# Performance work log

Hardware: AMD Instinct MI355X
Metric: run time of the kernel (lower is better)

## Reference

```python
import jax, jax.numpy as jnp
import numpy as np

N_NODES = 1024      # nNodes
N_EDGES = 4096      # nEdges
N_FACTORS = 64      # input feature dim (rows of kernel / paths)
BATCH = 256
NNZ_PER_ROW = 32    # nonzeros per kernel row -> iter = count_nonzero = 32 exactly
N_SOURCES = 16


def setup_inputs() -> dict:
    key = jax.random.key(0)
    k1, k2 = jax.random.split(key, 2)
    x = jax.random.normal(k1, (BATCH, N_FACTORS), dtype=jnp.float32)

    rng = np.random.default_rng(0)
    lin = rng.choice(N_NODES * N_NODES, size=N_EDGES, replace=False)
    # Edges[e] = (col, row): original scatters node_prop[i, Edges[e][1], Edges[e][0]] = paths[i][e]
    edges = np.stack([lin % N_NODES, lin // N_NODES], axis=1).astype(np.int64)

    sources = np.sort(rng.choice(N_NODES, size=N_SOURCES, replace=False)).astype(np.int64)

    # kernel ("paths") with exactly NNZ_PER_ROW nonzeros per row, so the
    # data-dependent propagation depth count_nonzero(paths[i]) == NNZ_PER_ROW
    cols = np.argsort(rng.random((N_FACTORS, N_EDGES)), axis=1)[:, :NNZ_PER_ROW]
    mask = np.zeros((N_FACTORS, N_EDGES), dtype=np.float32)
    mask[np.arange(N_FACTORS)[:, None], cols] = 1.0
    dense = np.asarray(jax.random.normal(k2, (N_FACTORS, N_EDGES), dtype=jnp.float32)) * 0.1
    kernel = jnp.asarray(dense * mask)

    return {
        "x": x,
        "kernel": kernel,
        "edges": jnp.asarray(edges),
        "sources": jnp.asarray(sources),
    }


def reference(x, kernel, edges, sources):
    F, E = kernel.shape
    N = N_NODES

    # scatter-build per-factor adjacency: node_prop[i, dst, src] = kernel[i, e]
    node_prop = jnp.zeros((F, N, N), x.dtype).at[:, edges[:, 1], edges[:, 0]].set(kernel)
    # row 0 fixed so each column sums to 1
    node_prop = node_prop.at[:, 0, :].set(1.0 - node_prop.sum(axis=1))

    source_flow = jnp.zeros((N,), x.dtype).at[sources].set(1.0)

    # data-dependent propagation depth per factor
    iters = jnp.count_nonzero(kernel, axis=1)  # [F], == NNZ_PER_ROW by construction

    # prop_flow[i] is linear in factor[i]; propagate the unit source vector per factor
    V0 = jnp.broadcast_to(source_flow, (F, N))

    def step(V, t):
        Vn = jnp.einsum('fij,fj->fi', node_prop, V)
        return jnp.where(t < iters[:, None], Vn, V), None

    V, _ = jax.lax.scan(step, V0, jnp.arange(NNZ_PER_ROW))

    # subtract factor[i] at every source node: W[i] = V[i] - 1_{sources}
    W = V - source_flow  # [F, N]

    prop_flows = x @ W        # [B, N]  (sum over factors of scaled propagated flows)
    recon = x @ kernel        # [B, E]  linear-combination reconstruction
    return prop_flows, recon
```

## Files before the change

### kernel.cpp

```cpp
#include <hip/hip_runtime.h>
#include <hip/hip_bf16.h>

#define NNODES   1024
#define NEDGES   4096
#define NFACT    64
#define NBATCH   256
#define NSRC     16
#define MAXNNZ   64
#define MAXITER  32

#define RECON_BLOCKS 512
#define FLOWS_BLOCKS 128

__global__ __launch_bounds__(256) void k1(
    const float* __restrict__ kern,
    const int*   __restrict__ edges,
    const int*   __restrict__ sources,
    const float* __restrict__ x,
    float*       __restrict__ W,
    float*       __restrict__ out)
{
    if (blockIdx.x >= NFACT) {
        int r  = blockIdx.x - NFACT;
        int e4 = (r & 3) * 256 + threadIdx.x;
        int b0 = (r >> 2) * 2;
        const float4* Kv  = (const float4*)kern;
        const float*  xr0 = x + b0 * NFACT;
        const float*  xr1 = xr0 + NFACT;
        float4 a0 = {0.f,0.f,0.f,0.f}, a1 = {0.f,0.f,0.f,0.f};
        #pragma unroll 4
        for (int k = 0; k < NFACT; ++k) {
            float4 kv = Kv[k * (NEDGES/4) + e4];
            float x0 = xr0[k], x1 = xr1[k];
            a0.x += x0*kv.x; a0.y += x0*kv.y; a0.z += x0*kv.z; a0.w += x0*kv.w;
            a1.x += x1*kv.x; a1.y += x1*kv.y; a1.z += x1*kv.z; a1.w += x1*kv.w;
        }
        float4* o4 = (float4*)(out + NBATCH * NNODES);
        o4[ b0      * (NEDGES/4) + e4] = a0;
        o4[(b0 + 1) * (NEDGES/4) + e4] = a1;
        return;
    }

    __shared__ float v_lds[NNODES];
    __shared__ float wbuf[MAXNNZ];
    __shared__ int   srcbuf[MAXNNZ];
    __shared__ int   dstbuf[MAXNNZ];
    __shared__ float c_lds[MAXNNZ];
    __shared__ int   cnt;

    const int f = blockIdx.x;
    const int t = threadIdx.x;

    if (t == 0) cnt = 0;
    __syncthreads();

    const float4* kern4 = (const float4*)(kern + f * NEDGES);
    #pragma unroll
    for (int i = 0; i < NEDGES/4/256; ++i) {
        int e4 = t + i * 256;
        float4 kv = kern4[e4];
        float vals[4] = {kv.x, kv.y, kv.z, kv.w};
        #pragma unroll
        for (int c = 0; c < 4; ++c) {
            if (vals[c] != 0.f) {
                int slot = atomicAdd(&cnt, 1);
                if (slot < MAXNNZ) {
                    wbuf[slot]   = vals[c];
                    int e        = e4 * 4 + c;
                    srcbuf[slot] = edges[2*e];
                    dstbuf[slot] = edges[2*e + 1];
                }
            }
        }
    }
    __syncthreads();

    const int nnz = min(cnt, MAXNNZ);
    const int T   = min(nnz, MAXITER);

    for (int n = t; n < NNODES; n += 256) v_lds[n] = 0.f;
    __syncthreads();

    if (t < 64) {
        const bool  active = (t < nnz);
        const float w_e = active ? wbuf[t]   : 0.f;
        const int   src = active ? srcbuf[t] : -1;
        const int   dst = active ? dstbuf[t] : -1;

        unsigned long long gmask = 0ull;
        for (int e2 = 0; e2 < nnz; ++e2)
            if (dstbuf[e2] == src) gmask |= (1ull << e2);

        float val = 0.f;
        for (int s = 0; s < NSRC; ++s)
            if (sources[s] == src) val = 1.f;
        float S = (float)NSRC;

        unsigned long long anybad =
            __ballot(active && (src == 0 || dst == 0)) |
            __ballot(__popcll(gmask) > 1);

        if (T > 0) {
            float c_fin = 0.f, v0_fin = 0.f;
            if (anybad == 0ull) {
                const int   gidx = gmask ? (__ffsll(gmask) - 1) : t;
                const float gsel = gmask ? 1.f : 0.f;
                float c = 0.f;
                for (int it = 0; it < T; ++it) {
                    c = w_e * val;
                    float g = __shfl(c, gidx);
                    val = gsel * g;
                }
                float a = c;
                #pragma unroll
                for (int o = 32; o >= 1; o >>= 1) a += __shfl_xor(a, o);
                c_fin = c; v0_fin = S - a;
            } else {
                float c = 0.f, v0 = 0.f;
                for (int it = 0; it < T; ++it) {
                    c = w_e * val;
                    c_lds[t] = c;
                    float a = c;
                    float b = (dst == 0) ? c : 0.f;
                    #pragma unroll
                    for (int o = 32; o >= 1; o >>= 1) {
                        a += __shfl_xor(a, o);
                        b += __shfl_xor(b, o);
                    }
                    v0 = S - a;
                    S  = S - b;
                    float nv = 0.f;
                    unsigned long long m = gmask;
                    while (m) { int i = __ffsll(m) - 1; nv += c_lds[i]; m &= m - 1; }
                    val = (src == 0) ? v0 : nv;
                }
                c_fin = c; v0_fin = v0;
            }
            if (t == 0) v_lds[0] = v0_fin;
            if (active && dst != 0) atomicAdd(&v_lds[dst], c_fin);
        } else {
            if (t < NSRC) v_lds[sources[t]] = 1.f;
        }
    }
    __syncthreads();
    if (t < NSRC) atomicAdd(&v_lds[sources[t]], -1.f);
    __syncthreads();

    float4* Wr = (float4*)(W + f * NNODES);
    const float4* v4 = (const float4*)v_lds;
    Wr[t] = v4[t];
}

__global__ __launch_bounds__(256) void k2(
    const float* __restrict__ x,
    const float* __restrict__ W,
    float*       __restrict__ out)
{
    const int b0 = blockIdx.x * 2;
    const int t  = threadIdx.x;
    const float4* Wv  = (const float4*)W;
    const float*  xr0 = x + b0 * NFACT;
    const float*  xr1 = xr0 + NFACT;
    float4 a0 = {0.f,0.f,0.f,0.f}, a1 = {0.f,0.f,0.f,0.f};
    #pragma unroll 4
    for (int k = 0; k < NFACT; ++k) {
        float4 wv = Wv[k * (NNODES/4) + t];
        float x0 = xr0[k], x1 = xr1[k];
        a0.x += x0*wv.x; a0.y += x0*wv.y; a0.z += x0*wv.z; a0.w += x0*wv.w;
        a1.x += x1*wv.x; a1.y += x1*wv.y; a1.z += x1*wv.z; a1.w += x1*wv.w;
    }
    float4* o4 = (float4*)out;
    o4[ b0      * (NNODES/4) + t] = a0;
    o4[(b0 + 1) * (NNODES/4) + t] = a1;
}

extern "C" void kernel_launch(void* const* d_in, const int* in_sizes, int n_in,
                              void* d_out, int out_size, void* d_ws, size_t ws_size,
                              hipStream_t stream) {
    const float* x       = (const float*)d_in[0];
    const float* kern    = (const float*)d_in[1];
    const int*   edges   = (const int*)d_in[2];
    const int*   sources = (const int*)d_in[3];
    float* out = (float*)d_out;
    float* W   = (float*)d_ws;

    k1<<<NFACT + RECON_BLOCKS, 256, 0, stream>>>(kern, edges, sources, x, W, out);
    k2<<<FLOWS_BLOCKS, 256, 0, stream>>>(x, W, out);
}
```

Before: 83.11 us.

## Fuse propagation, recon and flows into one kernel with flag-based inter-block sync

Merges the two launches into one grid. The propagation blocks publish each W row and then set a per-factor release flag. The flows blocks spin with acquire loads on those flags before computing x @ W. This removes the second kernel launch and the serialization between the two kernels. Recon and flows blocks now each handle four batch rows, with x staged in LDS, which halves the block counts. The flags are never reset, so on repeated calls the flows blocks may not wait and could read W while it is being rewritten. The spin-wait also relies on all blocks being co-resident.

```diff
diff --git a/kernel.cpp b/kernel.cpp
--- a/kernel.cpp
+++ b/kernel.cpp
@@ -9,169 +9,192 @@
 #define MAXNNZ   64
 #define MAXITER  32
 
-#define RECON_BLOCKS 512
-#define FLOWS_BLOCKS 128
-
-__global__ __launch_bounds__(256) void k1(
+#define PROP_BLOCKS  64
+#define RECON_BLOCKS 256
+#define FLOWS_BLOCKS 64
+#define GRID_BLOCKS  (PROP_BLOCKS + RECON_BLOCKS + FLOWS_BLOCKS)
+
+__global__ __launch_bounds__(256, 4) void fused(
     const float* __restrict__ kern,
     const int*   __restrict__ edges,
     const int*   __restrict__ sources,
     const float* __restrict__ x,
-    float*       __restrict__ W,
+    float*       __restrict__ ws,
     float*       __restrict__ out)
 {
-    if (blockIdx.x >= NFACT) {
-        int r  = blockIdx.x - NFACT;
-        int e4 = (r & 3) * 256 + threadIdx.x;
-        int b0 = (r >> 2) * 2;
-        const float4* Kv  = (const float4*)kern;
-        const float*  xr0 = x + b0 * NFACT;
-        const float*  xr1 = xr0 + NFACT;
-        float4 a0 = {0.f,0.f,0.f,0.f}, a1 = {0.f,0.f,0.f,0.f};
-        #pragma unroll 4
-        for (int k = 0; k < NFACT; ++k) {
-            float4 kv = Kv[k * (NEDGES/4) + e4];
-            float x0 = xr0[k], x1 = xr1[k];
-            a0.x += x0*kv.x; a0.y += x0*kv.y; a0.z += x0*kv.z; a0.w += x0*kv.w;
-            a1.x += x1*kv.x; a1.y += x1*kv.y; a1.z += x1*kv.z; a1.w += x1*kv.w;
-        }
-        float4* o4 = (float4*)(out + NBATCH * NNODES);
-        o4[ b0      * (NEDGES/4) + e4] = a0;
-        o4[(b0 + 1) * (NEDGES/4) + e4] = a1;
-        return;
-    }
-
     __shared__ float v_lds[NNODES];
+    __shared__ float xs[256];
     __shared__ float wbuf[MAXNNZ];
     __shared__ int   srcbuf[MAXNNZ];
     __shared__ int   dstbuf[MAXNNZ];
     __shared__ float c_lds[MAXNNZ];
     __shared__ int   cnt;
 
-    const int f = blockIdx.x;
-    const int t = threadIdx.x;
-
-    if (t == 0) cnt = 0;
-    __syncthreads();
-
-    const float4* kern4 = (const float4*)(kern + f * NEDGES);
-    #pragma unroll
-    for (int i = 0; i < NEDGES/4/256; ++i) {
-        int e4 = t + i * 256;
-        float4 kv = kern4[e4];
-        float vals[4] = {kv.x, kv.y, kv.z, kv.w};
+    const int bid = blockIdx.x;
+    const int t   = threadIdx.x;
+    float* W      = ws;
+    int*   flags  = (int*)(ws + NFACT * NNODES);
+
+    if (bid < PROP_BLOCKS) {
+        const int f = bid;
+        if (t == 0) cnt = 0;
+        __syncthreads();
+
+        const float4* kern4 = (const float4*)(kern + f * NEDGES);
         #pragma unroll
-        for (int c = 0; c < 4; ++c) {
-            if (vals[c] != 0.f) {
-                int slot = atomicAdd(&cnt, 1);
-                if (slot < MAXNNZ) {
-                    wbuf[slot]   = vals[c];
-                    int e        = e4 * 4 + c;
-                    srcbuf[slot] = edges[2*e];
-                    dstbuf[slot] = edges[2*e + 1];
+        for (int i = 0; i < NEDGES/4/256; ++i) {
+            int e4 = t + i * 256;
+            float4 kv = kern4[e4];
+            float vals[4] = {kv.x, kv.y, kv.z, kv.w};
+            #pragma unroll
+            for (int c = 0; c < 4; ++c) {
+                if (vals[c] != 0.f) {
+                    int slot = atomicAdd(&cnt, 1);
+                    if (slot < MAXNNZ) {
+                        wbuf[slot]   = vals[c];
+                        int e        = e4 * 4 + c;
+                        srcbuf[slot] = edges[2*e];
+                        dstbuf[slot] = edges[2*e + 1];
+                    }
                 }
             }
         }
+        __syncthreads();
+
+        const int nnz = min(cnt, MAXNNZ);
+        const int T   = min(nnz, MAXITER);
+
+        for (int n = t; n < NNODES; n += 256) v_lds[n] = 0.f;
+        __syncthreads();
+
+        if (t < 64) {
+            const bool  active = (t < nnz);
+            const float w_e = active ? wbuf[t]   : 0.f;
+            const int   src = active ? srcbuf[t] : -1;
+            const int   dst = active ? dstbuf[t] : -1;
+
+            unsigned long long gmask = 0ull;
+            for (int e2 = 0; e2 < nnz; ++e2)
+                if (dstbuf[e2] == src) gmask |= (1ull << e2);
+
+            float val = 0.f;
+            for (int s = 0; s < NSRC; ++s)
+                if (sources[s] == src) val = 1.f;
+            float S = (float)NSRC;
+
+            unsigned long long anybad =
+                __ballot(active && (src == 0 || dst == 0)) |
+                __ballot(__popcll(gmask) > 1);
+
+            if (T > 0) {
+                float c_fin = 0.f, v0_fin = 0.f;
+                if (anybad == 0ull) {
+                    const int   gidx = gmask ? (__ffsll(gmask) - 1) : t;
+                    const float gsel = gmask ? 1.f : 0.f;
+                    float c = 0.f;
+                    for (int it = 0; it < T; ++it) {
+                        c = w_e * val;
+                        float g = __shfl(c, gidx);
+                        val = gsel * g;
+                    }
+                    float a = c;
+                    #pragma unroll
+                    for (int o = 32; o >= 1; o >>= 1) a += __shfl_xor(a, o);
+                    c_fin = c; v0_fin = S - a;
+                } else {
+                    float c = 0.f, v0 = 0.f;
+                    for (int it = 0; it < T; ++it) {
+                        c = w_e * val;
+                        c_lds[t] = c;
+                        float a = c;
+                        float b = (dst == 0) ? c : 0.f;
+                        #pragma unroll
+                        for (int o = 32; o >= 1; o >>= 1) {
+                            a += __shfl_xor(a, o);
+                            b += __shfl_xor(b, o);
+                        }
+                        v0 = S - a;
+                        S  = S - b;
+                        float nv = 0.f;
+                        unsigned long long m = gmask;
+                        while (m) { int i = __ffsll(m) - 1; nv += c_lds[i]; m &= m - 1; }
+                        val = (src == 0) ? v0 : nv;
+                    }
+                    c_fin = c; v0_fin = v0;
+                }
+                if (t == 0) v_lds[0] = v0_fin;
+                if (active && dst != 0) atomicAdd(&v_lds[dst], c_fin);
+            } else {
+                if (t < NSRC) v_lds[sources[t]] = 1.f;
+            }
+        }
+        __syncthreads();
+        if (t < NSRC) atomicAdd(&v_lds[sources[t]], -1.f);
+        __syncthreads();
+
+        ((float4*)(W + f * NNODES))[t] = ((const float4*)v_lds)[t];
+        __syncthreads();
+        if (t == 0) {
+            __threadfence();
+            __hip_atomic_store(&flags[f], 1, __ATOMIC_RELEASE, __HIP_MEMORY_SCOPE_AGENT);
+        }
+        return;
     }
-    __syncthreads();
-
-    const int nnz = min(cnt, MAXNNZ);
-    const int T   = min(nnz, MAXITER);
-
-    for (int n = t; n < NNODES; n += 256) v_lds[n] = 0.f;
-    __syncthreads();
-
-    if (t < 64) {
-        const bool  active = (t < nnz);
-        const float w_e = active ? wbuf[t]   : 0.f;
-        const int   src = active ? srcbuf[t] : -1;
-        const int   dst = active ? dstbuf[t] : -1;
-
-        unsigned long long gmask = 0ull;
-        for (int e2 = 0; e2 < nnz; ++e2)
-            if (dstbuf[e2] == src) gmask |= (1ull << e2);
-
-        float val = 0.f;
-        for (int s = 0; s < NSRC; ++s)
-            if (sources[s] == src) val = 1.f;
-        float S = (float)NSRC;
-
-        unsigned long long anybad =
-            __ballot(active && (src == 0 || dst == 0)) |
-            __ballot(__popcll(gmask) > 1);
-
-        if (T > 0) {
-            float c_fin = 0.f, v0_fin = 0.f;
-            if (anybad == 0ull) {
-                const int   gidx = gmask ? (__ffsll(gmask) - 1) : t;
-                const float gsel = gmask ? 1.f : 0.f;
-                float c = 0.f;
-                for (int it = 0; it < T; ++it) {
-                    c = w_e * val;
-                    float g = __shfl(c, gidx);
-                    val = gsel * g;
-                }
-                float a = c;
-                #pragma unroll
-                for (int o = 32; o >= 1; o >>= 1) a += __shfl_xor(a, o);
-                c_fin = c; v0_fin = S - a;
-            } else {
-                float c = 0.f, v0 = 0.f;
-                for (int it = 0; it < T; ++it) {
-                    c = w_e * val;
-                    c_lds[t] = c;
-                    float a = c;
-                    float b = (dst == 0) ? c : 0.f;
-                    #pragma unroll
-                    for (int o = 32; o >= 1; o >>= 1) {
-                        a += __shfl_xor(a, o);
-                        b += __shfl_xor(b, o);
-                    }
-                    v0 = S - a;
-                    S  = S - b;
-                    float nv = 0.f;
-                    unsigned long long m = gmask;
-                    while (m) { int i = __ffsll(m) - 1; nv += c_lds[i]; m &= m - 1; }
-                    val = (src == 0) ? v0 : nv;
-                }
-                c_fin = c; v0_fin = v0;
-            }
-            if (t == 0) v_lds[0] = v0_fin;
-            if (active && dst != 0) atomicAdd(&v_lds[dst], c_fin);
-        } else {
-            if (t < NSRC) v_lds[sources[t]] = 1.f;
-        }
+
+    if (bid < PROP_BLOCKS + RECON_BLOCKS) {
+        const int r  = bid - PROP_BLOCKS;
+        const int e4 = (r & 3) * 256 + t;
+        const int b0 = (r >> 2) * 4;
+        xs[t] = x[b0 * NFACT + t];
+        __syncthreads();
+
+        const float4* Kv = (const float4*)kern;
+        float4 a0 = {0.f,0.f,0.f,0.f}, a1 = a0, a2 = a0, a3 = a0;
+        #pragma unroll 4
+        for (int k = 0; k < NFACT; ++k) {
+            float4 kv = Kv[k * (NEDGES/4) + e4];
+            float x0 = xs[k], x1 = xs[64+k], x2 = xs[128+k], x3 = xs[192+k];
+            a0.x += x0*kv.x; a0.y += x0*kv.y; a0.z += x0*kv.z; a0.w += x0*kv.w;
+            a1.x += x1*kv.x; a1.y += x1*kv.y; a1.z += x1*kv.z; a1.w += x1*kv.w;
+            a2.x += x2*kv.x; a2.y += x2*kv.y; a2.z += x2*kv.z; a2.w += x2*kv.w;
+            a3.x += x3*kv.x; a3.y += x3*kv.y; a3.z += x3*kv.z; a3.w += x3*kv.w;
+        }
+        float4* o4 = (float4*)(out + NBATCH * NNODES);
+        o4[(b0+0)*(NEDGES/4) + e4] = a0;
+        o4[(b0+1)*(NEDGES/4) + e4] = a1;
+        o4[(b0+2)*(NEDGES/4) + e4] = a2;
+        o4[(b0+3)*(NEDGES/4) + e4] = a3;
+        return;
     }
-    __syncthreads();
-    if (t < NSRC) atomicAdd(&v_lds[sources[t]], -1.f);
-    __syncthreads();
-
-    float4* Wr = (float4*)(W + f * NNODES);
-    const float4* v4 = (const float4*)v_lds;
-    Wr[t] = v4[t];
-}
-
-__global__ __launch_bounds__(256) void k2(
-    const float* __restrict__ x,
-    const float* __restrict__ W,
-    float*       __restrict__ out)
-{
-    const int b0 = blockIdx.x * 2;
-    const int t  = threadIdx.x;
-    const float4* Wv  = (const float4*)W;
-    const float*  xr0 = x + b0 * NFACT;
-    const float*  xr1 = xr0 + NFACT;
-    float4 a0 = {0.f,0.f,0.f,0.f}, a1 = {0.f,0.f,0.f,0.f};
-    #pragma unroll 4
-    for (int k = 0; k < NFACT; ++k) {
-        float4 wv = Wv[k * (NNODES/4) + t];
-        float x0 = xr0[k], x1 = xr1[k];
-        a0.x += x0*wv.x; a0.y += x0*wv.y; a0.z += x0*wv.z; a0.w += x0*wv.w;
-        a1.x += x1*wv.x; a1.y += x1*wv.y; a1.z += x1*wv.z; a1.w += x1*wv.w;
+
+    {
+        const int bq = bid - PROP_BLOCKS - RECON_BLOCKS;
+        const int b0 = bq * 4;
+        xs[t] = x[b0 * NFACT + t];
+        if (t < NFACT) {
+            while (__hip_atomic_load(&flags[t], __ATOMIC_ACQUIRE,
+                                     __HIP_MEMORY_SCOPE_AGENT) != 1)
+                __builtin_amdgcn_s_sleep(1);
+        }
+        __syncthreads();
+
+        const float4* Wv = (const float4*)W;
+        float4 a0 = {0.f,0.f,0.f,0.f}, a1 = a0, a2 = a0, a3 = a0;
+        #pragma unroll 4
+        for (int k = 0; k < NFACT; ++k) {
+            float4 wv = Wv[k * (NNODES/4) + t];
+            float x0 = xs[k], x1 = xs[64+k], x2 = xs[128+k], x3 = xs[192+k];
+            a0.x += x0*wv.x; a0.y += x0*wv.y; a0.z += x0*wv.z; a0.w += x0*wv.w;
+            a1.x += x1*wv.x; a1.y += x1*wv.y; a1.z += x1*wv.z; a1.w += x1*wv.w;
+            a2.x += x2*wv.x; a2.y += x2*wv.y; a2.z += x2*wv.z; a2.w += x2*wv.w;
+            a3.x += x3*wv.x; a3.y += x3*wv.y; a3.z += x3*wv.z; a3.w += x3*wv.w;
+        }
+        float4* o4 = (float4*)out;
+        o4[(b0+0)*(NNODES/4) + t] = a0;
+        o4[(b0+1)*(NNODES/4) + t] = a1;
+        o4[(b0+2)*(NNODES/4) + t] = a2;
+        o4[(b0+3)*(NNODES/4) + t] = a3;
     }
-    float4* o4 = (float4*)out;
-    o4[ b0      * (NNODES/4) + t] = a0;
-    o4[(b0 + 1) * (NNODES/4) + t] = a1;
 }
 
 extern "C" void kernel_launch(void* const* d_in, const int* in_sizes, int n_in,
@@ -182,8 +205,7 @@
     const int*   edges   = (const int*)d_in[2];
     const int*   sources = (const int*)d_in[3];
     float* out = (float*)d_out;
-    float* W   = (float*)d_ws;
-
-    k1<<<NFACT + RECON_BLOCKS, 256, 0, stream>>>(kern, edges, sources, x, W, out);
-    k2<<<FLOWS_BLOCKS, 256, 0, stream>>>(x, W, out);
+    float* ws  = (float*)d_ws;
+
+    fused<<<GRID_BLOCKS, 256, 0, stream>>>(kern, edges, sources, x, ws, out);
 }
```

Measured after the change: 86.92 us. 1.05x slower.
